# Optimization experiments

Measured on AMD Instinct MI355X. Metric: run time of the kernel, lower is better.

Reference implementation:

```python
import jax, jax.numpy as jnp
import numpy as np

B, S = 2, 1024
ENC_IN, MARK_IN = 21, 4
PRED_LEN, C_OUT = 96, 21
E = 512                 # embedding_dim
INNER = 2 * E           # proj_factor=2.0 (library default; Model does not pass it)
NH = 8                  # mLSTM heads
DH = INNER // NH        # 128
K = 4                   # causal conv1d kernel
BS = 4                  # qkv_proj_blocksize
NHP = INNER // BS       # 256 block-diagonal proj heads
NB = 4                  # num_blocks
EPS = 1e-5


def setup_inputs() -> dict:
    key = jax.random.key(0)
    ks = jax.random.split(key, 24)
    it = iter(range(24))
    def n(shape, s=0.02):
        return jax.random.normal(ks[next(it)], shape, jnp.float32) * s
    return {
        "x_enc": n((B, S, ENC_IN), 1.0),
        "x_mark_enc": n((B, S, MARK_IN), 1.0),
        "x_dec": n((B, PRED_LEN, ENC_IN), 1.0),
        "x_mark_dec": n((B, PRED_LEN, MARK_IN), 1.0),
        "emb_W": n((ENC_IN + MARK_IN, E), 0.05),
        "emb_b": jnp.zeros((E,), jnp.float32),
        "ln_w": jnp.ones((NB, E), jnp.float32),
        "up_W": n((NB, E, 2 * INNER)),
        "conv_W": n((NB, INNER, K), 0.1),
        "conv_b": jnp.zeros((NB, INNER), jnp.float32),
        "q_W": n((NB, NHP, BS, BS), 0.1),
        "k_W": n((NB, NHP, BS, BS), 0.1),
        "v_W": n((NB, NHP, BS, BS), 0.1),
        "ig_W": n((NB, 3 * INNER, NH)),
        "ig_b": jnp.zeros((NB, NH), jnp.float32),
        "fg_W": n((NB, 3 * INNER, NH)),
        "fg_b": jnp.tile(jnp.linspace(3.0, 6.0, NH, dtype=jnp.float32), (NB, 1)),
        "skip": jnp.ones((NB, INNER), jnp.float32),
        "onorm_w": jnp.ones((NB, INNER), jnp.float32),
        "down_W": n((NB, INNER, E)),
        "post_ln_w": jnp.ones((E,), jnp.float32),
        "head_W": n((E, C_OUT), 0.05),
        "head_b": jnp.zeros((C_OUT,), jnp.float32),
    }


def _ln(x, w):
    mu = jnp.mean(x, -1, keepdims=True)
    var = jnp.var(x, -1, keepdims=True)
    return (x - mu) * jax.lax.rsqrt(var + EPS) * w


def _headwise(x, w):
    # block-diagonal LinearHeadwiseExpand: (B,S,INNER) with (NHP,BS,BS) blocks
    xh = x.reshape(x.shape[0], x.shape[1], NHP, BS)
    return jnp.einsum('bshd,hod->bsho', xh, w).reshape(x.shape)


def _block(x, lw, uW, cW, cb, qW, kW, vW, igW, igb, fgW, fgb, sk, ow, dW):
    xn = _ln(x, lw)
    up = xn @ uW                                  # (B,S,2*INNER)
    xm, z = up[..., :INNER], up[..., INNER:]
    # causal depthwise conv1d + SiLU
    xc = jax.lax.conv_general_dilated(
        xm.transpose(0, 2, 1), cW[:, None, :], (1,), [(K - 1, 0)],
        feature_group_count=INNER,
        dimension_numbers=('NCH', 'OIH', 'NCH')).transpose(0, 2, 1) + cb
    xc = jax.nn.silu(xc)
    q = _headwise(xc, qW)
    k = _headwise(xc, kW)
    v = _headwise(xm, vW)
    qkv = jnp.concatenate([q, k, v], -1)          # (B,S,3*INNER)
    ig = (qkv @ igW + igb).transpose(0, 2, 1)     # (B,NH,S)
    fg = (qkv @ fgW + fgb).transpose(0, 2, 1)
    qh = q.reshape(B, S, NH, DH).transpose(0, 2, 1, 3)
    kh = k.reshape(B, S, NH, DH).transpose(0, 2, 1, 3)
    vh = v.reshape(B, S, NH, DH).transpose(0, 2, 1, 3)
    # parallel stabilized mLSTM (exp-gated linear attention)
    log_f = jax.nn.log_sigmoid(fg)
    cs = jnp.cumsum(log_f, -1)                    # (B,NH,S)
    Mmat = cs[..., :, None] - cs[..., None, :]    # (B,NH,S,S) cumulative decay
    tri = jnp.tril(jnp.ones((S, S), bool))
    logD = jnp.where(tri, Mmat + ig[..., None, :], -jnp.inf)
    m = jnp.max(logD, -1, keepdims=True)          # row-wise stabilizer
    D = jnp.exp(logD - m)
    qk = jnp.einsum('bnsd,bntd->bnst', qh, kh) / (DH ** 0.5)
    C = qk * D
    norm = jnp.maximum(jnp.abs(jnp.sum(C, -1, keepdims=True)), jnp.exp(-m))
    h = jnp.einsum('bnst,bntd->bnsd', C / (norm + 1e-6), vh)
    # multi-head layernorm (groupnorm over DH per head), weight, no bias
    hn = (h - jnp.mean(h, -1, keepdims=True)) * jax.lax.rsqrt(jnp.var(h, -1, keepdims=True) + EPS)
    hn = hn.transpose(0, 2, 1, 3).reshape(B, S, INNER) * ow
    hs = (hn + sk * xc) * jax.nn.silu(z)          # learnable skip + output gate
    return x + hs @ dW                            # residual


def reference(x_enc, x_mark_enc, x_dec, x_mark_dec, emb_W, emb_b, ln_w, up_W,
              conv_W, conv_b, q_W, k_W, v_W, ig_W, ig_b, fg_W, fg_b, skip,
              onorm_w, down_W, post_ln_w, head_W, head_b):
    x = jnp.concatenate([x_enc, x_mark_enc], -1) @ emb_W + emb_b
    for i in range(NB):
        x = _block(x, ln_w[i], up_W[i], conv_W[i], conv_b[i], q_W[i], k_W[i],
                   v_W[i], ig_W[i], ig_b[i], fg_W[i], fg_b[i], skip[i],
                   onorm_w[i], down_W[i])
    x = _ln(x, post_ln_w)
    return x[:, -PRED_LEN:, :] @ head_W + head_b
```

## Files before the change

kernel.cpp:

```cpp
#include <hip/hip_runtime.h>
#include <hip/hip_bf16.h>

#define S_LEN 1024
#define E_DIM 512
#define INNER_D 1024
#define NHEAD 8
#define DHEAD 128

typedef unsigned short u16;
typedef unsigned int u32;
typedef __attribute__((ext_vector_type(8))) short short8;
typedef __attribute__((ext_vector_type(4))) float f32x4;

union S8 { short8 v; u16 u[8]; uint4 q; };

__device__ __forceinline__ u16 f2bf(float f) {
  u32 u = __float_as_uint(f);
  u32 r = u + 0x7FFFu + ((u >> 16) & 1u);
  return (u16)(r >> 16);
}
__device__ __forceinline__ float bf2f(u16 u) { return __uint_as_float(((u32)u) << 16); }

__device__ __forceinline__ void gload16(const u16* g, u16* l) {
  __builtin_amdgcn_global_load_lds((const __attribute__((address_space(1))) void*)g,
                                   (__attribute__((address_space(3))) void*)l, 16, 0, 0);
}

__device__ __forceinline__ void prep_transpose(
    const float* __restrict__ in, u16* __restrict__ out, int K, int N,
    int k0, int n0, int t, u16 (*T)[72])
{
  int kr = t >> 2, nseg = (t & 3) * 16;
  const float* src = in + (size_t)(k0 + kr) * N + n0 + nseg;
#pragma unroll
  for (int j = 0; j < 16; j++) T[kr][nseg + j] = f2bf(src[j]);
  __syncthreads();
  int nr = t >> 2, kseg = (t & 3) * 16;
  u32 u[8];
#pragma unroll
  for (int rr = 0; rr < 8; rr++) {
    u32 lo = T[kseg + 2 * rr][nr];
    u32 hi = T[kseg + 2 * rr + 1][nr];
    u[rr] = lo | (hi << 16);
  }
  u16* dst = out + (size_t)(n0 + nr) * K + k0 + kseg;
  uint4 w0 = {u[0], u[1], u[2], u[3]};
  uint4 w1 = {u[4], u[5], u[6], u[7]};
  *(uint4*)dst = w0;
  *(uint4*)(dst + 8) = w1;
}

__global__ __launch_bounds__(256) void prep_kernel(
    const float* __restrict__ up_W, u16* __restrict__ upWt,
    const float* __restrict__ down_W, u16* __restrict__ dnWt,
    const float* __restrict__ igW, const float* __restrict__ fgW,
    u16* __restrict__ ghi, u16* __restrict__ glo,
    const float* __restrict__ xe, const float* __restrict__ xmk,
    const float* __restrict__ eW, const float* __restrict__ eb,
    float* __restrict__ x)
{
  __shared__ u16 T[64][72];
  __shared__ float in_s[25];
  int id = blockIdx.x;
  int t = threadIdx.x;
  if (id < 1024) {
    int bx = id & 7, rest = id >> 3;
    int by = rest & 31, L = rest >> 5;
    prep_transpose(up_W + (size_t)L * 512 * 2048, upWt + (size_t)L * 1048576,
                   512, 2048, bx * 64, by * 64, t, T);
  } else if (id < 1536) {
    int id2 = id - 1024;
    int bx = id2 & 15, rest = id2 >> 4;
    int by = rest & 7, L = rest >> 3;
    prep_transpose(down_W + (size_t)L * 1024 * 512, dnWt + (size_t)L * 524288,
                   1024, 512, bx * 64, by * 64, t, T);
  } else if (id < 2304) {
    int id3 = id - 1536;
    int bx = id3 % 12, rest = id3 / 12;
    int n = rest & 15, L = rest >> 4;
    int k = bx * 256 + t;
    const float* W = ((n < 8) ? igW : fgW) + (size_t)L * 24576;
    float v = W[(size_t)k * 8 + (n & 7)];
    u16 h = f2bf(v);
    u16 l = f2bf(v - bf2f(h));
    size_t o = ((size_t)L * 16 + n) * 3072 + k;
    ghi[o] = h;
    glo[o] = l;
  } else {
    int row = id - 2304;
    if (t < 21) in_s[t] = xe[row * 21 + t];
    else if (t < 25) in_s[t] = xmk[row * 4 + t - 21];
    __syncthreads();
#pragma unroll
    for (int rep = 0; rep < 2; rep++) {
      int e = t + rep * 256;
      float acc = eb[e];
#pragma unroll
      for (int i = 0; i < 25; i++) acc += in_s[i] * eW[i * E_DIM + e];
      x[(size_t)row * E_DIM + e] = acc;
    }
  }
}

__global__ __launch_bounds__(256) void ln_kernel(
    const float* __restrict__ x, const float* __restrict__ w, u16* __restrict__ out)
{
  int row = blockIdx.x, tid = threadIdx.x;
  const float* xr = x + (size_t)row * E_DIM;
  float2 v = *(const float2*)(xr + tid * 2);
  float s = v.x + v.y, q = v.x * v.x + v.y * v.y;
#pragma unroll
  for (int off = 32; off; off >>= 1) { s += __shfl_xor(s, off); q += __shfl_xor(q, off); }
  __shared__ float ssum[4], ssq[4];
  int wv = tid >> 6;
  if ((tid & 63) == 0) { ssum[wv] = s; ssq[wv] = q; }
  __syncthreads();
  s = ssum[0] + ssum[1] + ssum[2] + ssum[3];
  q = ssq[0] + ssq[1] + ssq[2] + ssq[3];
  float mu = s * (1.f / E_DIM);
  float var = q * (1.f / E_DIM) - mu * mu;
  float rs = rsqrtf(var + 1e-5f);
  int e = tid * 2;
  ushort2 o;
  o.x = f2bf((v.x - mu) * rs * w[e]);
  o.y = f2bf((v.y - mu) * rs * w[e + 1]);
  *(ushort2*)(out + (size_t)row * E_DIM + e) = o;
}

__global__ __launch_bounds__(256) void lnhead_kernel(
    const float* __restrict__ x, const float* __restrict__ w,
    const float* __restrict__ hW, const float* __restrict__ hb,
    float* __restrict__ out)
{
  int ridx = blockIdx.x;
  int b = ridx / 96, r = ridx % 96;
  int row = b * S_LEN + (S_LEN - 96) + r;
  int tid = threadIdx.x;
  const float* xr = x + (size_t)row * E_DIM;
  float2 v = *(const float2*)(xr + tid * 2);
  float s = v.x + v.y, q = v.x * v.x + v.y * v.y;
#pragma unroll
  for (int off = 32; off; off >>= 1) { s += __shfl_xor(s, off); q += __shfl_xor(q, off); }
  __shared__ float ssum[4], ssq[4];
  __shared__ float lnv[512];
  __shared__ float part[8][32];
  int wv = tid >> 6;
  if ((tid & 63) == 0) { ssum[wv] = s; ssq[wv] = q; }
  __syncthreads();
  s = ssum[0] + ssum[1] + ssum[2] + ssum[3];
  q = ssq[0] + ssq[1] + ssq[2] + ssq[3];
  float mu = s * (1.f / E_DIM);
  float var = q * (1.f / E_DIM) - mu * mu;
  float rs = rsqrtf(var + 1e-5f);
  int e = tid * 2;
  lnv[e]     = (v.x - mu) * rs * w[e];
  lnv[e + 1] = (v.y - mu) * rs * w[e + 1];
  __syncthreads();
  int n = tid & 31, sl = tid >> 5;
  float p = 0.f;
  if (n < 21) {
#pragma unroll 8
    for (int kk = 0; kk < 64; kk++)
      p += lnv[sl * 64 + kk] * hW[(sl * 64 + kk) * 21 + n];
  }
  part[sl][n] = p;
  __syncthreads();
  if (tid < 21) {
    float acc = hb[tid];
#pragma unroll
    for (int j = 0; j < 8; j++) acc += part[j][tid];
    out[ridx * 21 + tid] = acc;
  }
}

__global__ __launch_bounds__(256) void gemm_bf16_split64(
    const u16* __restrict__ A, const u16* __restrict__ Bt,
    float* __restrict__ C0, u16* __restrict__ C1,
    int M, int N, int K, int split_col, int ldc)
{
  __shared__ u16 As0[128 * 32], As1[128 * 32], As2[128 * 32];
  __shared__ u16 Bs0[128 * 32], Bs1[128 * 32], Bs2[128 * 32];
  const int tid = threadIdx.x;
  const int row0 = blockIdx.y * 128, col0 = blockIdx.x * 128;
  const int wave = tid >> 6, lane = tid & 63;
  const int wr = wave >> 1, wc = wave & 1;
  const int lm = lane & 15, lq = lane >> 4;
  const int lr4 = lane >> 2;
  const int cg4 = (lane & 3) ^ (lr4 & 3);
  f32x4 acc[4][4] = {};
  const u16* Abase = A + (size_t)(row0 + lr4) * K + cg4 * 8;
  const u16* Bbase = Bt + (size_t)(col0 + lr4) * K + cg4 * 8;
  const int key = lm & 3;

#define STG_UP(AS, BS, K0) do { \
  _Pragma("unroll") for (int i = 0; i < 2; i++) \
    gload16(Abase + (size_t)((wave * 2 + i) * 16) * K + (K0), &AS[(wave * 2 + i) * 512]); \
  _Pragma("unroll") for (int i = 0; i < 2; i++) \
    gload16(Bbase + (size_t)((wave * 2 + i) * 16) * K + (K0), &BS[(wave * 2 + i) * 512]); \
} while (0)

#define CMP_UP(AS, BS) do { \
  short8 af[4], bfv[4]; \
  _Pragma("unroll") for (int i = 0; i < 4; i++) \
    af[i] = *(const short8*)&AS[(wr * 64 + i * 16 + lm) * 32 + ((lq ^ key) * 8)]; \
  _Pragma("unroll") for (int j = 0; j < 4; j++) \
    bfv[j] = *(const short8*)&BS[(wc * 64 + j * 16 + lm) * 32 + ((lq ^ key) * 8)]; \
  _Pragma("unroll") for (int i = 0; i < 4; i++) \
    _Pragma("unroll") for (int j = 0; j < 4; j++) \
      acc[i][j] = __builtin_amdgcn_mfma_f32_16x16x32_bf16(af[i], bfv[j], acc[i][j], 0, 0, 0); \
} while (0)

  STG_UP(As0, Bs0, 0);
  asm volatile("" ::: "memory");
  STG_UP(As1, Bs1, 32);
  asm volatile("" ::: "memory");
  STG_UP(As2, Bs2, 64);
#pragma unroll
  for (int t = 0; t < 16; t++) {
    if (t <= 13)      asm volatile("s_waitcnt vmcnt(8)" ::: "memory");
    else if (t == 14) asm volatile("s_waitcnt vmcnt(4)" ::: "memory");
    else              asm volatile("s_waitcnt vmcnt(0)" ::: "memory");
    __builtin_amdgcn_sched_barrier(0);
    __builtin_amdgcn_s_barrier();
    if ((t % 3) == 0)      CMP_UP(As0, Bs0);
    else if ((t % 3) == 1) CMP_UP(As1, Bs1);
    else                   CMP_UP(As2, Bs2);
    __builtin_amdgcn_s_barrier();
    if (t + 3 < 16) {
      if ((t % 3) == 0)      STG_UP(As0, Bs0, (t + 3) * 32);
      else if ((t % 3) == 1) STG_UP(As1, Bs1, (t + 3) * 32);
      else                   STG_UP(As2, Bs2, (t + 3) * 32);
    }
  }
#undef STG_UP
#undef CMP_UP

  const bool toC1 = (col0 >= split_col);
#pragma unroll
  for (int i = 0; i < 4; i++) {
#pragma unroll
    for (int j = 0; j < 4; j++) {
      int col = col0 - (toC1 ? split_col : 0) + wc * 64 + j * 16 + lm;
#pragma unroll
      for (int r = 0; r < 4; r++) {
        int row = row0 + wr * 64 + i * 16 + lq * 4 + r;
        if (toC1) C1[(size_t)row * ldc + col] = f2bf(acc[i][j][r]);
        else C0[(size_t)row * ldc + col] = acc[i][j][r];
      }
    }
  }
}

__global__ __launch_bounds__(256) void gemm_bf16_32(
    const u16* __restrict__ A, const u16* __restrict__ Bt,
    float* __restrict__ C, int M, int N, int K, int ldc)
{
  __shared__ u16 As0[64 * 64], As1[64 * 64], As2[64 * 64];
  __shared__ u16 Bs0[64 * 64], Bs1[64 * 64], Bs2[64 * 64];
  const int tid = threadIdx.x;
  const int row0 = blockIdx.y * 64, col0 = blockIdx.x * 64;
  const int wave = tid >> 6, lane = tid & 63;
  const int wr = wave >> 1, wc = wave & 1;
  const int lm = lane & 15, lq = lane >> 4;
  const int lr = lane >> 3;
  const int cg = (lane & 7) ^ lr;
  f32x4 acc[2][2] = {};
  const u16* Abase = A + (size_t)(row0 + lr) * K + cg * 8;
  const u16* Bbase = Bt + (size_t)(col0 + lr) * K + cg * 8;
  const int key = lm & 7;

#define STAGE_DN(AS, BS, K0) do { \
  _Pragma("unroll") for (int i = 0; i < 2; i++) \
    gload16(Abase + (size_t)((wave * 2 + i) * 8) * K + (K0), &AS[(wave * 2 + i) * 512]); \
  _Pragma("unroll") for (int j = 0; j < 2; j++) \
    gload16(Bbase + (size_t)((wave * 2 + j) * 8) * K + (K0), &BS[(wave * 2 + j) * 512]); \
} while (0)

#define COMPUTE_DN(AS, BS) do { \
  short8 af[2][2], bfv[2][2]; \
  _Pragma("unroll") for (int kc = 0; kc < 2; kc++) { \
    _Pragma("unroll") for (int i = 0; i < 2; i++) \
      af[kc][i] = *(const short8*)&AS[(wr * 32 + i * 16 + lm) * 64 + (((kc * 4 + lq) ^ key) * 8)]; \
    _Pragma("unroll") for (int j = 0; j < 2; j++) \
      bfv[kc][j] = *(const short8*)&BS[(wc * 32 + j * 16 + lm) * 64 + (((kc * 4 + lq) ^ key) * 8)]; \
  } \
  _Pragma("unroll") for (int kc = 0; kc < 2; kc++) \
    _Pragma("unroll") for (int i = 0; i < 2; i++) \
      _Pragma("unroll") for (int j = 0; j < 2; j++) \
        acc[i][j] = __builtin_amdgcn_mfma_f32_16x16x32_bf16(af[kc][i], bfv[kc][j], acc[i][j], 0, 0, 0); \
} while (0)

  STAGE_DN(As0, Bs0, 0);
  asm volatile("" ::: "memory");
  STAGE_DN(As1, Bs1, 64);
  asm volatile("" ::: "memory");
  STAGE_DN(As2, Bs2, 128);
#pragma unroll
  for (int t = 0; t < 16; t++) {
    if (t <= 13)      asm volatile("s_waitcnt vmcnt(8)" ::: "memory");
    else if (t == 14) asm volatile("s_waitcnt vmcnt(4)" ::: "memory");
    else              asm volatile("s_waitcnt vmcnt(0)" ::: "memory");
    __builtin_amdgcn_sched_barrier(0);
    __builtin_amdgcn_s_barrier();
    if ((t % 3) == 0)      COMPUTE_DN(As0, Bs0);
    else if ((t % 3) == 1) COMPUTE_DN(As1, Bs1);
    else                   COMPUTE_DN(As2, Bs2);
    __builtin_amdgcn_s_barrier();
    if (t + 3 < 16) {
      if ((t % 3) == 0)      STAGE_DN(As0, Bs0, (t + 3) * 64);
      else if ((t % 3) == 1) STAGE_DN(As1, Bs1, (t + 3) * 64);
      else                   STAGE_DN(As2, Bs2, (t + 3) * 64);
    }
  }
#undef STAGE_DN
#undef COMPUTE_DN

#pragma unroll
  for (int i = 0; i < 2; i++) {
#pragma unroll
    for (int j = 0; j < 2; j++) {
      int col = col0 + wc * 32 + j * 16 + lm;
#pragma unroll
      for (int r = 0; r < 4; r++) {
        int row = row0 + wr * 32 + i * 16 + lq * 4 + r;
        C[(size_t)row * ldc + col] += acc[i][j][r];
      }
    }
  }
}

__global__ __launch_bounds__(256) void convqkv_kernel(
    const float* __restrict__ xm,
    const float* __restrict__ cw, const float* __restrict__ cb,
    const float* __restrict__ qw, const float* __restrict__ kw, const float* __restrict__ vw,
    float* __restrict__ xc, u16* __restrict__ q, u16* __restrict__ k, u16* __restrict__ v,
    u16* __restrict__ vt)
{
  int r0 = blockIdx.x * 8;
  int s0 = r0 & (S_LEN - 1);
  int g = threadIdx.x;
  int c0 = g * 4;
  const float* base = xm + (size_t)r0 * INNER_D + c0;

  float4 xv[11];
#pragma unroll
  for (int j = 0; j < 11; j++) {
    int ts = s0 - 3 + j;
    float4 t = {0.f, 0.f, 0.f, 0.f};
    if (ts >= 0) t = *(const float4*)(base + (ptrdiff_t)(j - 3) * INNER_D);
    xv[j] = t;
  }
  float cwv[4][4];
#pragma unroll
  for (int c = 0; c < 4; c++)
#pragma unroll
    for (int kk = 0; kk < 4; kk++) cwv[c][kk] = cw[(c0 + c) * 4 + kk];
  float cbv[4] = {cb[c0], cb[c0 + 1], cb[c0 + 2], cb[c0 + 3]};
  const float* qg = qw + g * 16;
  const float* kg = kw + g * 16;
  const float* vg = vw + g * 16;
  float qwv[16], kwv[16], vwv[16];
#pragma unroll
  for (int i = 0; i < 16; i++) { qwv[i] = qg[i]; kwv[i] = kg[i]; vwv[i] = vg[i]; }

  u32 vt_pack[4][4];

#pragma unroll
  for (int i = 0; i < 8; i++) {
    float a0 = cbv[0], a1 = cbv[1], a2 = cbv[2], a3 = cbv[3];
#pragma unroll
    for (int kk = 0; kk < 4; kk++) {
      float4 xvv = xv[i + kk];
      a0 += xvv.x * cwv[0][kk];
      a1 += xvv.y * cwv[1][kk];
      a2 += xvv.z * cwv[2][kk];
      a3 += xvv.w * cwv[3][kk];
    }
    a0 = a0 / (1.f + __expf(-a0));
    a1 = a1 / (1.f + __expf(-a1));
    a2 = a2 / (1.f + __expf(-a2));
    a3 = a3 / (1.f + __expf(-a3));
    float4 accv = {a0, a1, a2, a3};
    *(float4*)(xc + (size_t)(r0 + i) * INNER_D + c0) = accv;

    float xcv[4] = {a0, a1, a2, a3};
    float xmv[4] = {xv[i + 3].x, xv[i + 3].y, xv[i + 3].z, xv[i + 3].w};
    ushort4 qs, ks, vs;
    u16* qp = (u16*)&qs; u16* kp = (u16*)&ks; u16* vp = (u16*)&vs;
#pragma unroll
    for (int o = 0; o < 4; o++) {
      float aq = 0.f, ak = 0.f, av = 0.f;
#pragma unroll
      for (int d = 0; d < 4; d++) {
        aq += xcv[d] * qwv[o * 4 + d];
        ak += xcv[d] * kwv[o * 4 + d];
        av += xmv[d] * vwv[o * 4 + d];
      }
      qp[o] = f2bf(aq); kp[o] = f2bf(ak);
      u16 vv = f2bf(av);
      vp[o] = vv;
      if ((i & 1) == 0) vt_pack[o][i >> 1] = (u32)vv;
      else              vt_pack[o][i >> 1] |= ((u32)vv) << 16;
    }
    size_t off = (size_t)(r0 + i) * INNER_D + c0;
    *(ushort4*)(q + off) = qs;
    *(ushort4*)(k + off) = ks;
    *(ushort4*)(v + off) = vs;
  }
  u16* vtb = vt + ((size_t)((r0 >> 10) * INNER_D + c0)) * S_LEN + s0;
#pragma unroll
  for (int c = 0; c < 4; c++) {
    uint4 wv4 = {vt_pack[c][0], vt_pack[c][1], vt_pack[c][2], vt_pack[c][3]};
    *(uint4*)(vtb + (size_t)c * S_LEN) = wv4;
  }
}

__global__ __launch_bounds__(256) void gates_mfma_kernel(
    const u16* __restrict__ q, const u16* __restrict__ k, const u16* __restrict__ v,
    const u16* __restrict__ whi, const u16* __restrict__ wlo,
    const float* __restrict__ igb, const float* __restrict__ fgb,
    float* __restrict__ ig, float* __restrict__ fg)
{
  const int blk2 = blockIdx.x;
  const int blk = blk2 >> 1, half = blk2 & 1;
  const int tid = threadIdx.x;
  const int wave = tid >> 6, lane = tid & 63;
  const int lm = lane & 15, lq = lane >> 4;
  const int grow = blk * 16 + lm;
  const u16* parts[3] = {q, k, v};
  f32x4 acc = {};
#pragma unroll 4
  for (int kc = 0; kc < 12; kc++) {
    int k0 = half * 1536 + wave * 384 + kc * 32;
    int part = k0 >> 10;
    int idx = (k0 & 1023) + lq * 8;
    S8 a, bh_, bl_;
    a.q = *(const uint4*)(parts[part] + (size_t)grow * INNER_D + idx);
    bh_.q = *(const uint4*)(whi + (size_t)lm * 3072 + k0 + lq * 8);
    bl_.q = *(const uint4*)(wlo + (size_t)lm * 3072 + k0 + lq * 8);
    __builtin_amdgcn_s_setprio(1);
    acc = __builtin_amdgcn_mfma_f32_16x16x32_bf16(a.v, bh_.v, acc, 0, 0, 0);
    acc = __builtin_amdgcn_mfma_f32_16x16x32_bf16(a.v, bl_.v, acc, 0, 0, 0);
    __builtin_amdgcn_s_setprio(0);
  }
  __shared__ float red[4][16][17];
#pragma unroll
  for (int r = 0; r < 4; r++) red[wave][lq * 4 + r][lm] = acc[r];
  __syncthreads();
  if (wave == 0) {
#pragma unroll
    for (int r = 0; r < 4; r++) {
      int row = lq * 4 + r;
      float sum = red[0][row][lm] + red[1][row][lm] + red[2][row][lm] + red[3][row][lm];
      int growr = blk * 16 + row;
      int b = growr >> 10, s = growr & (S_LEN - 1);
      if (lm < 8) {
        float bias = (half == 0) ? igb[lm] : 0.f;
        ig[half * 16384 + ((size_t)(b * NHEAD + lm) << 10) + s] = sum + bias;
      } else {
        float bias = (half == 0) ? fgb[lm - 8] : 0.f;
        fg[half * 16384 + ((size_t)(b * NHEAD + (lm - 8)) << 10) + s] = sum + bias;
      }
    }
  }
}

__global__ __launch_bounds__(1024) void scan_kernel(
    const float* __restrict__ ig, const float* __restrict__ fg,
    float* __restrict__ a, float* __restrict__ rm, float* __restrict__ enm)
{
  int bh = blockIdx.x;
  int t = threadIdx.x;
  int lane = t & 63, wv = t >> 6;
  __shared__ float sw[16];
  size_t o = ((size_t)bh << 10) + t;
  float f = fg[o] + fg[16384 + o];
  float lf = (f >= 0.f) ? -log1pf(__expf(-f)) : f - log1pf(__expf(f));
  float v = lf;
#pragma unroll
  for (int off = 1; off < 64; off <<= 1) {
    float u = __shfl_up(v, off);
    if (lane >= off) v += u;
  }
  if (lane == 63) sw[wv] = v;
  __syncthreads();
  float pre = 0.f;
  for (int w = 0; w < wv; w++) pre += sw[w];
  float cs = v + pre;
  float av = (ig[o] + ig[16384 + o]) - cs;
  a[o] = __expf(av);
  float m = av;
#pragma unroll
  for (int off = 1; off < 64; off <<= 1) {
    float u = __shfl_up(m, off);
    if (lane >= off) m = fmaxf(m, u);
  }
  __syncthreads();
  if (lane == 63) sw[wv] = m;
  __syncthreads();
  float pm = -3.4e38f;
  for (int w = 0; w < wv; w++) pm = fmaxf(pm, sw[w]);
  float rmx = fmaxf(m, pm);
  rm[o] = rmx;
  enm[o] = __expf(-(cs + rmx));
}

__device__ __constant__ int c_qp[15] = {7, 7, 7, 6, 6, 6, 5, 5, 4, 4, 3, 3, 2, 1, 0};
__device__ __constant__ int c_k0[15] = {0, 6,11, 0, 5,10, 0, 6, 0, 5, 0, 4, 0, 0, 0};
__device__ __constant__ int c_k1[15] = {6,11,16, 5,10,14, 6,12, 5,10, 4, 8, 6, 4, 2};
__device__ __constant__ int c_md[15] = {1, 2, 3, 1, 2, 3, 1, 2, 1, 2, 1, 2, 0, 0, 0};

#define HP_SLOT 1310720
#define SC_SLOT 10240

__global__ __launch_bounds__(512) void attn_mfma_kernel(
    const u16* __restrict__ qhg, const u16* __restrict__ khg, const u16* __restrict__ vtg,
    const float* __restrict__ a_arr, const float* __restrict__ rm_arr, const float* __restrict__ enm_arr,
    const float* __restrict__ xc, const u16* __restrict__ zh,
    const float* __restrict__ skip, const float* __restrict__ onw,
    u16* __restrict__ hs, float* __restrict__ hpart, float* __restrict__ scpart)
{
  const int bh = blockIdx.x;
  const int job = blockIdx.y;
  const int qp = c_qp[job], k0t = c_k0[job], k1t = c_k1[job], mode = c_md[job];
  const int b = bh >> 3, h = bh & 7;
  const int s0 = qp * 128;
  const int tid = threadIdx.x;
  const int wave = tid >> 6, lane = tid & 63;
  const int lm = lane & 15, lq = lane >> 4;
  const size_t rowbase = (size_t)b * S_LEN;
  const int c0 = h * DHEAD;

  __shared__ u16 Ks0[64 * 128], Ks1[64 * 128];
  __shared__ u16 Vt0[128 * 64], Vt1[128 * 64];
  __shared__ u16 Ws[128 * 72];

  short8 aq[4];
  {
    const u16* qpp = qhg + (rowbase + s0 + wave * 16 + lm) * INNER_D + c0 + lq * 8;
#pragma unroll
    for (int kc = 0; kc < 4; kc++) {
      S8 tmp; tmp.q = *(const uint4*)(qpp + kc * 32);
      aq[kc] = tmp.v;
    }
  }
  const float scale = 0.08838834764831845f;
  float rmv[4], er[4];
#pragma unroll
  for (int r = 0; r < 4; r++) {
    rmv[r] = rm_arr[(size_t)bh * S_LEN + s0 + wave * 16 + lq * 4 + r];
    er[r] = scale * __expf(-rmv[r]);
  }

  f32x4 accH[8] = {};
  float sc_acc[4] = {0.f, 0.f, 0.f, 0.f};
  const int lr16 = lane >> 4;
  const int ls16 = lane & 15;
  const int lr8 = lane >> 3;
  const int cgv = (lane & 7) ^ lr8;
  const u16* vtbase = vtg + ((size_t)b * INNER_D + c0) * S_LEN;

  float ae0[4], ae1[4];

#define PREF(KS, VS, AE, T0) do { \
  _Pragma("unroll") for (int j = 0; j < 2; j++) { \
    int rK = (wave * 2 + j) * 4 + lr16; \
    int cgk = ls16 ^ (rK & 7); \
    gload16(khg + (rowbase + (T0) + rK) * INNER_D + c0 + cgk * 8, &KS[(wave * 2 + j) * 512]); \
  } \
  _Pragma("unroll") for (int j = 0; j < 2; j++) { \
    int rV = (wave * 2 + j) * 8 + lr8; \
    gload16(vtbase + (size_t)rV * S_LEN + (T0) + cgv * 8, &VS[(wave * 2 + j) * 512]); \
  } \
  _Pragma("unroll") for (int cb = 0; cb < 4; cb++) \
    AE[cb] = a_arr[(size_t)bh * S_LEN + (T0) + cb * 16 + lm]; \
} while (0)

#define QK_STEP(KS, PACC) do { \
  __builtin_amdgcn_s_setprio(1); \
  _Pragma("unroll") for (int kc = 0; kc < 4; kc++) \
    _Pragma("unroll") for (int cb = 0; cb < 4; cb++) { \
      short8 bk = *(const short8*)&KS[(cb * 16 + lm) * 128 + (((kc * 4 + lq) ^ (lm & 7)) * 8)]; \
      PACC[cb] = __builtin_amdgcn_mfma_f32_16x16x32_bf16(aq[kc], bk, PACC[cb], 0, 0, 0); \
    } \
  __builtin_amdgcn_s_setprio(0); \
} while (0)

#define W_PV(AE, VT, T0, PACC) do { \
  float wpart[4] = {0.f, 0.f, 0.f, 0.f}; \
  _Pragma("unroll") for (int cb = 0; cb < 4; cb++) { \
    int colg = (T0) + cb * 16 + lm; \
    float ec = AE[cb]; \
    _Pragma("unroll") for (int r = 0; r < 4; r++) { \
      int rowg = s0 + wave * 16 + lq * 4 + r; \
      float wv = PACC[cb][r] * ec * er[r]; \
      if (colg > rowg) wv = 0.f; \
      wpart[r] += wv; \
      Ws[(wave * 16 + lq * 4 + r) * 72 + cb * 16 + lm] = f2bf(wv); \
    } \
  } \
  _Pragma("unroll") for (int r = 0; r < 4; r++) { \
    float sr = wpart[r]; \
    sr += __shfl_xor(sr, 1); sr += __shfl_xor(sr, 2); \
    sr += __shfl_xor(sr, 4); sr += __shfl_xor(sr, 8); \
    sc_acc[r] += sr; \
  } \
  __builtin_amdgcn_s_setprio(1); \
  _Pragma("unroll") for (int kc = 0; kc < 2; kc++) { \
    short8 aw = *(const short8*)&Ws[(wave * 16 + lm) * 72 + kc * 32 + lq * 8]; \
    _Pragma("unroll") for (int nb = 0; nb < 8; nb++) { \
      short8 bv = *(const short8*)&VT[(nb * 16 + lm) * 64 + (((kc * 4 + lq) ^ (lm & 7)) * 8)]; \
      accH[nb] = __builtin_amdgcn_mfma_f32_16x16x32_bf16(aw, bv, accH[nb], 0, 0, 0); \
    } \
  } \
  __builtin_amdgcn_s_setprio(0); \
} while (0)

  int kt = k0t;
  PREF(Ks0, Vt0, ae0, kt * 64);
  asm volatile("" ::: "memory");
  if (kt + 1 < k1t) PREF(Ks1, Vt1, ae1, (kt + 1) * 64);

  while (true) {
    {
      if (kt + 1 < k1t) asm volatile("s_waitcnt vmcnt(8)" ::: "memory");
      else              asm volatile("s_waitcnt vmcnt(0)" ::: "memory");
      __builtin_amdgcn_sched_barrier(0);
      __builtin_amdgcn_s_barrier();
      f32x4 pacc[4] = {};
      QK_STEP(Ks0, pacc);
      W_PV(ae0, Vt0, kt * 64, pacc);
      __builtin_amdgcn_s_barrier();
      if (kt + 2 < k1t) PREF(Ks0, Vt0, ae0, (kt + 2) * 64);
      kt++;
      if (kt >= k1t) break;
    }
    {
      if (kt + 1 < k1t) asm volatile("s_waitcnt vmcnt(8)" ::: "memory");
      else              asm volatile("s_waitcnt vmcnt(0)" ::: "memory");
      __builtin_amdgcn_sched_barrier(0);
      __builtin_amdgcn_s_barrier();
      f32x4 pacc[4] = {};
      QK_STEP(Ks1, pacc);
      W_PV(ae1, Vt1, kt * 64, pacc);
      __builtin_amdgcn_s_barrier();
      if (kt + 2 < k1t) PREF(Ks1, Vt1, ae1, (kt + 2) * 64);
      kt++;
      if (kt >= k1t) break;
    }
  }
#undef PREF
#undef QK_STEP
#undef W_PV

  if (mode != 0) {
    int slot = mode - 1;
    int qr = qp - 3;
    float* Hp = hpart + (size_t)slot * HP_SLOT + ((size_t)(bh * 5 + qr)) * 16384;
    float* sp = scpart + slot * SC_SLOT + (bh * 5 + qr) * 128;
#pragma unroll
    for (int r = 0; r < 4; r++) {
      int row = wave * 16 + lq * 4 + r;
      if (lm == 0) sp[row] = sc_acc[r];
#pragma unroll
      for (int nb = 0; nb < 8; nb++)
        Hp[row * 128 + nb * 16 + lm] = accH[nb][r];
    }
    return;
  }

  float inv[4], muv[4], rsv[4];
#pragma unroll
  for (int r = 0; r < 4; r++) {
    int rowg = s0 + wave * 16 + lq * 4 + r;
    float nrm = fmaxf(fabsf(sc_acc[r]), enm_arr[(size_t)bh * S_LEN + rowg]);
    inv[r] = 1.f / (nrm + 1e-6f);
  }
#pragma unroll
  for (int r = 0; r < 4; r++) {
    float s = 0.f, qq = 0.f;
#pragma unroll
    for (int nb = 0; nb < 8; nb++) {
      float hv = accH[nb][r] * inv[r];
      accH[nb][r] = hv;
      s += hv; qq += hv * hv;
    }
    s += __shfl_xor(s, 1); s += __shfl_xor(s, 2); s += __shfl_xor(s, 4); s += __shfl_xor(s, 8);
    qq += __shfl_xor(qq, 1); qq += __shfl_xor(qq, 2); qq += __shfl_xor(qq, 4); qq += __shfl_xor(qq, 8);
    float mu = s * (1.f / DHEAD);
    float var = qq * (1.f / DHEAD) - mu * mu;
    muv[r] = mu;
    rsv[r] = rsqrtf(var + 1e-5f);
  }
  float ow[8], sk[8];
#pragma unroll
  for (int nb = 0; nb < 8; nb++) {
    ow[nb] = onw[c0 + nb * 16 + lm];
    sk[nb] = skip[c0 + nb * 16 + lm];
  }
#pragma unroll
  for (int r = 0; r < 4; r++) {
    int rowg = s0 + wave * 16 + lq * 4 + r;
    size_t base = (rowbase + rowg) * INNER_D + c0;
#pragma unroll
    for (int nb = 0; nb < 8; nb++) {
      int d = nb * 16 + lm;
      float xcv = xc[base + d];
      float zv = bf2f(zh[base + d]);
      float hn = (accH[nb][r] - muv[r]) * rsv[r] * ow[nb] + sk[nb] * xcv;
      float o = hn * (zv / (1.f + __expf(-zv)));
      hs[base + d] = f2bf(o);
    }
  }
}

__global__ __launch_bounds__(256) void attn_combine_kernel(
    const float* __restrict__ hpart, const float* __restrict__ scpart,
    const float* __restrict__ enm,
    const float* __restrict__ xc, const u16* __restrict__ zh,
    const float* __restrict__ skip, const float* __restrict__ onw,
    u16* __restrict__ hs)
{
  int wave = threadIdx.x >> 6, lane = threadIdx.x & 63;
  int gid = blockIdx.x * 4 + wave;
  int bh = gid / 640;
  int rr = gid % 640;
  int qr = rr >> 7, row = rr & 127;
  int b = bh >> 3, hh = bh & 7;
  int s = (qr + 3) * 128 + row;
  int nsl = (qr >= 3) ? 3 : 2;
  size_t off = (((size_t)(bh * 5 + qr)) * 128 + row) * 128 + lane * 2;
  int sidx = (bh * 5 + qr) * 128 + row;
  float hx = 0.f, hy = 0.f, sc = 0.f;
  for (int sl = 0; sl < nsl; sl++) {
    float2 hp = *(const float2*)(hpart + (size_t)sl * HP_SLOT + off);
    hx += hp.x; hy += hp.y;
    sc += scpart[sl * SC_SLOT + sidx];
  }
  float nrm = fmaxf(fabsf(sc), enm[(size_t)bh * S_LEN + s]);
  float inv = 1.f / (nrm + 1e-6f);
  hx *= inv; hy *= inv;
  float sm = hx + hy, sq = hx * hx + hy * hy;
#pragma unroll
  for (int off2 = 32; off2; off2 >>= 1) { sm += __shfl_xor(sm, off2); sq += __shfl_xor(sq, off2); }
  float mu = sm * (1.f / DHEAD);
  float var = sq * (1.f / DHEAD) - mu * mu;
  float rs = rsqrtf(var + 1e-5f);
  int c0 = hh * DHEAD + lane * 2;
  size_t base = ((size_t)(b * S_LEN + s)) * INNER_D + c0;
  float2 xc2 = *(const float2*)(xc + base);
  ushort2 z2u = *(const ushort2*)(zh + base);
  float z2x = bf2f(z2u.x), z2y = bf2f(z2u.y);
  float skx = skip[c0], sky = skip[c0 + 1];
  float owx = onw[c0],  owy = onw[c0 + 1];
  ushort2 o;
  o.x = f2bf(((hx - mu) * rs * owx + skx * xc2.x) * (z2x / (1.f + __expf(-z2x))));
  o.y = f2bf(((hy - mu) * rs * owy + sky * xc2.y) * (z2y / (1.f + __expf(-z2y))));
  *(ushort2*)(hs + base) = o;
}

extern "C" void kernel_launch(void* const* d_in, const int* in_sizes, int n_in,
                              void* d_out, int out_size, void* d_ws, size_t ws_size,
                              hipStream_t stream)
{
  const float* x_enc   = (const float*)d_in[0];
  const float* x_mark  = (const float*)d_in[1];
  const float* emb_W   = (const float*)d_in[4];
  const float* emb_b   = (const float*)d_in[5];
  const float* ln_w    = (const float*)d_in[6];
  const float* up_W    = (const float*)d_in[7];
  const float* conv_W  = (const float*)d_in[8];
  const float* conv_b  = (const float*)d_in[9];
  const float* q_W     = (const float*)d_in[10];
  const float* k_W     = (const float*)d_in[11];
  const float* v_W     = (const float*)d_in[12];
  const float* ig_W    = (const float*)d_in[13];
  const float* ig_b    = (const float*)d_in[14];
  const float* fg_W    = (const float*)d_in[15];
  const float* fg_b    = (const float*)d_in[16];
  const float* skip_w  = (const float*)d_in[17];
  const float* onorm_w = (const float*)d_in[18];
  const float* down_W  = (const float*)d_in[19];
  const float* post_ln = (const float*)d_in[20];
  const float* head_W  = (const float*)d_in[21];
  const float* head_b  = (const float*)d_in[22];

  float* p = (float*)d_ws;
  float* x    = p; p += 1048576;
  float* xm   = p; p += 2097152;
  float* xc   = p; p += 2097152;
  float* igb_ = p; p += 32768;
  float* fgb_ = p; p += 32768;
  float* ab   = p; p += 16384;
  float* rmb  = p; p += 16384;
  float* enmb = p; p += 16384;
  u16* qhb = (u16*)p; p += 1048576;
  u16* khb = (u16*)p; p += 1048576;
  u16* vhb = (u16*)p; p += 1048576;
  u16* zh  = (u16*)p; p += 1048576;
  u16* xnh = (u16*)p; p += 524288;
  u16* upWtA = (u16*)p; p += 2097152;
  u16* dnWtA = (u16*)p; p += 1048576;
  u16* gtwH = (u16*)p; p += 98304;
  u16* gtwL = (u16*)p; p += 98304;
  float* hpart = p; p += 3932160;
  float* scpart = p; p += 32768;
  u16* vtg = (u16*)p; p += 1048576;
  u16* hsbh = (u16*)xm;

  prep_kernel<<<4352, 256, 0, stream>>>(
      up_W, upWtA, down_W, dnWtA, ig_W, fg_W, gtwH, gtwL,
      x_enc, x_mark, emb_W, emb_b, x);

  for (int L = 0; L < 4; L++) {
    ln_kernel<<<2048, 256, 0, stream>>>(x, ln_w + L * 512, xnh);
    gemm_bf16_split64<<<dim3(16, 16), 256, 0, stream>>>(
        xnh, upWtA + (size_t)L * 1048576, xm, zh, 2048, 2048, 512, 1024, 1024);
    convqkv_kernel<<<256, 256, 0, stream>>>(
        xm, conv_W + L * 4096, conv_b + L * 1024,
        q_W + L * 4096, k_W + L * 4096, v_W + L * 4096,
        xc, qhb, khb, vhb, vtg);
    gates_mfma_kernel<<<256, 256, 0, stream>>>(
        qhb, khb, vhb, gtwH + (size_t)L * 49152, gtwL + (size_t)L * 49152,
        ig_b + L * 8, fg_b + L * 8, igb_, fgb_);
    scan_kernel<<<16, 1024, 0, stream>>>(igb_, fgb_, ab, rmb, enmb);
    attn_mfma_kernel<<<dim3(16, 15), 512, 0, stream>>>(
        qhb, khb, vtg, ab, rmb, enmb, xc, zh,
        skip_w + L * 1024, onorm_w + L * 1024, hsbh, hpart, scpart);
    attn_combine_kernel<<<2560, 256, 0, stream>>>(
        hpart, scpart, enmb, xc, zh, skip_w + L * 1024, onorm_w + L * 1024, hsbh);
    gemm_bf16_32<<<dim3(8, 32), 256, 0, stream>>>(
        hsbh, dnWtA + (size_t)L * 524288, x, 2048, 512, 1024, 512);
  }

  lnhead_kernel<<<192, 256, 0, stream>>>(x, post_ln, head_W, head_b, (float*)d_out);
}
```

Measured before the change: 428.8 us.

## Double GEMM K-tiles, compute mLSTM row sums via MFMA, skip mask on off-diagonal tiles

Both projection GEMMs now stage K-tiles twice as deep (64 and 128), with new XOR swizzles and half as many pipeline iterations and barriers. In the attention kernel, the per-row sum of the decay-weighted scores is computed with an extra MFMA against a ones vector, replacing the shuffle reductions. The causal mask is applied only on tiles that touch the diagonal. The row sum now uses bf16-rounded weights, which slightly changes the normaliser. The larger LDS footprint may reduce occupancy.

```diff
diff --git a/kernel.cpp b/kernel.cpp
--- a/kernel.cpp
+++ b/kernel.cpp
@@ -178,47 +178,49 @@
     float* __restrict__ C0, u16* __restrict__ C1,
     int M, int N, int K, int split_col, int ldc)
 {
-  __shared__ u16 As0[128 * 32], As1[128 * 32], As2[128 * 32];
-  __shared__ u16 Bs0[128 * 32], Bs1[128 * 32], Bs2[128 * 32];
+  __shared__ u16 As0[128 * 64], As1[128 * 64], As2[128 * 64];
+  __shared__ u16 Bs0[128 * 64], Bs1[128 * 64], Bs2[128 * 64];
   const int tid = threadIdx.x;
   const int row0 = blockIdx.y * 128, col0 = blockIdx.x * 128;
   const int wave = tid >> 6, lane = tid & 63;
   const int wr = wave >> 1, wc = wave & 1;
   const int lm = lane & 15, lq = lane >> 4;
-  const int lr4 = lane >> 2;
-  const int cg4 = (lane & 3) ^ (lr4 & 3);
+  const int lr8 = lane >> 3;
+  const int cg8 = (lane & 7) ^ lr8;
   f32x4 acc[4][4] = {};
-  const u16* Abase = A + (size_t)(row0 + lr4) * K + cg4 * 8;
-  const u16* Bbase = Bt + (size_t)(col0 + lr4) * K + cg4 * 8;
-  const int key = lm & 3;
+  const u16* Abase = A + (size_t)(row0 + lr8) * K + cg8 * 8;
+  const u16* Bbase = Bt + (size_t)(col0 + lr8) * K + cg8 * 8;
+  const int key = lm & 7;
 
 #define STG_UP(AS, BS, K0) do { \
-  _Pragma("unroll") for (int i = 0; i < 2; i++) \
-    gload16(Abase + (size_t)((wave * 2 + i) * 16) * K + (K0), &AS[(wave * 2 + i) * 512]); \
-  _Pragma("unroll") for (int i = 0; i < 2; i++) \
-    gload16(Bbase + (size_t)((wave * 2 + i) * 16) * K + (K0), &BS[(wave * 2 + i) * 512]); \
+  _Pragma("unroll") for (int i = 0; i < 4; i++) \
+    gload16(Abase + (size_t)((wave * 4 + i) * 8) * K + (K0), &AS[(wave * 4 + i) * 512]); \
+  _Pragma("unroll") for (int i = 0; i < 4; i++) \
+    gload16(Bbase + (size_t)((wave * 4 + i) * 8) * K + (K0), &BS[(wave * 4 + i) * 512]); \
 } while (0)
 
 #define CMP_UP(AS, BS) do { \
-  short8 af[4], bfv[4]; \
-  _Pragma("unroll") for (int i = 0; i < 4; i++) \
-    af[i] = *(const short8*)&AS[(wr * 64 + i * 16 + lm) * 32 + ((lq ^ key) * 8)]; \
-  _Pragma("unroll") for (int j = 0; j < 4; j++) \
-    bfv[j] = *(const short8*)&BS[(wc * 64 + j * 16 + lm) * 32 + ((lq ^ key) * 8)]; \
-  _Pragma("unroll") for (int i = 0; i < 4; i++) \
+  _Pragma("unroll") for (int kc = 0; kc < 2; kc++) { \
+    short8 af[4], bfv[4]; \
+    _Pragma("unroll") for (int i = 0; i < 4; i++) \
+      af[i] = *(const short8*)&AS[(wr * 64 + i * 16 + lm) * 64 + (((kc * 4 + lq) ^ key) * 8)]; \
     _Pragma("unroll") for (int j = 0; j < 4; j++) \
-      acc[i][j] = __builtin_amdgcn_mfma_f32_16x16x32_bf16(af[i], bfv[j], acc[i][j], 0, 0, 0); \
+      bfv[j] = *(const short8*)&BS[(wc * 64 + j * 16 + lm) * 64 + (((kc * 4 + lq) ^ key) * 8)]; \
+    _Pragma("unroll") for (int i = 0; i < 4; i++) \
+      _Pragma("unroll") for (int j = 0; j < 4; j++) \
+        acc[i][j] = __builtin_amdgcn_mfma_f32_16x16x32_bf16(af[i], bfv[j], acc[i][j], 0, 0, 0); \
+  } \
 } while (0)
 
   STG_UP(As0, Bs0, 0);
   asm volatile("" ::: "memory");
-  STG_UP(As1, Bs1, 32);
+  STG_UP(As1, Bs1, 64);
   asm volatile("" ::: "memory");
-  STG_UP(As2, Bs2, 64);
-#pragma unroll
-  for (int t = 0; t < 16; t++) {
-    if (t <= 13)      asm volatile("s_waitcnt vmcnt(8)" ::: "memory");
-    else if (t == 14) asm volatile("s_waitcnt vmcnt(4)" ::: "memory");
+  STG_UP(As2, Bs2, 128);
+#pragma unroll
+  for (int t = 0; t < 8; t++) {
+    if (t <= 5)       asm volatile("s_waitcnt vmcnt(16)" ::: "memory");
+    else if (t == 6)  asm volatile("s_waitcnt vmcnt(8)" ::: "memory");
     else              asm volatile("s_waitcnt vmcnt(0)" ::: "memory");
     __builtin_amdgcn_sched_barrier(0);
     __builtin_amdgcn_s_barrier();
@@ -226,10 +228,10 @@
     else if ((t % 3) == 1) CMP_UP(As1, Bs1);
     else                   CMP_UP(As2, Bs2);
     __builtin_amdgcn_s_barrier();
-    if (t + 3 < 16) {
-      if ((t % 3) == 0)      STG_UP(As0, Bs0, (t + 3) * 32);
-      else if ((t % 3) == 1) STG_UP(As1, Bs1, (t + 3) * 32);
-      else                   STG_UP(As2, Bs2, (t + 3) * 32);
+    if (t + 3 < 8) {
+      if ((t % 3) == 0)      STG_UP(As0, Bs0, (t + 3) * 64);
+      else if ((t % 3) == 1) STG_UP(As1, Bs1, (t + 3) * 64);
+      else                   STG_UP(As2, Bs2, (t + 3) * 64);
     }
   }
 #undef STG_UP
@@ -255,50 +257,52 @@
     const u16* __restrict__ A, const u16* __restrict__ Bt,
     float* __restrict__ C, int M, int N, int K, int ldc)
 {
-  __shared__ u16 As0[64 * 64], As1[64 * 64], As2[64 * 64];
-  __shared__ u16 Bs0[64 * 64], Bs1[64 * 64], Bs2[64 * 64];
+  __shared__ u16 As0[64 * 128], As1[64 * 128], As2[64 * 128];
+  __shared__ u16 Bs0[64 * 128], Bs1[64 * 128], Bs2[64 * 128];
   const int tid = threadIdx.x;
   const int row0 = blockIdx.y * 64, col0 = blockIdx.x * 64;
   const int wave = tid >> 6, lane = tid & 63;
   const int wr = wave >> 1, wc = wave & 1;
   const int lm = lane & 15, lq = lane >> 4;
-  const int lr = lane >> 3;
-  const int cg = (lane & 7) ^ lr;
+  const int lr16 = lane >> 4;
+  const int ls16 = lane & 15;
   f32x4 acc[2][2] = {};
-  const u16* Abase = A + (size_t)(row0 + lr) * K + cg * 8;
-  const u16* Bbase = Bt + (size_t)(col0 + lr) * K + cg * 8;
-  const int key = lm & 7;
 
 #define STAGE_DN(AS, BS, K0) do { \
-  _Pragma("unroll") for (int i = 0; i < 2; i++) \
-    gload16(Abase + (size_t)((wave * 2 + i) * 8) * K + (K0), &AS[(wave * 2 + i) * 512]); \
-  _Pragma("unroll") for (int j = 0; j < 2; j++) \
-    gload16(Bbase + (size_t)((wave * 2 + j) * 8) * K + (K0), &BS[(wave * 2 + j) * 512]); \
+  _Pragma("unroll") for (int i = 0; i < 4; i++) { \
+    int rA = (wave * 4 + i) * 4 + lr16; \
+    int cgk = ls16 ^ (rA & 15); \
+    gload16(A + (size_t)(row0 + rA) * K + (K0) + cgk * 8, &AS[(wave * 4 + i) * 512]); \
+  } \
+  _Pragma("unroll") for (int i = 0; i < 4; i++) { \
+    int rB = (wave * 4 + i) * 4 + lr16; \
+    int cgk = ls16 ^ (rB & 15); \
+    gload16(Bt + (size_t)(col0 + rB) * K + (K0) + cgk * 8, &BS[(wave * 4 + i) * 512]); \
+  } \
 } while (0)
 
 #define COMPUTE_DN(AS, BS) do { \
-  short8 af[2][2], bfv[2][2]; \
-  _Pragma("unroll") for (int kc = 0; kc < 2; kc++) { \
+  _Pragma("unroll") for (int kc = 0; kc < 4; kc++) { \
+    short8 af[2], bfv[2]; \
     _Pragma("unroll") for (int i = 0; i < 2; i++) \
-      af[kc][i] = *(const short8*)&AS[(wr * 32 + i * 16 + lm) * 64 + (((kc * 4 + lq) ^ key) * 8)]; \
+      af[i] = *(const short8*)&AS[(wr * 32 + i * 16 + lm) * 128 + (((kc * 4 + lq) ^ lm) * 8)]; \
     _Pragma("unroll") for (int j = 0; j < 2; j++) \
-      bfv[kc][j] = *(const short8*)&BS[(wc * 32 + j * 16 + lm) * 64 + (((kc * 4 + lq) ^ key) * 8)]; \
-  } \
-  _Pragma("unroll") for (int kc = 0; kc < 2; kc++) \
+      bfv[j] = *(const short8*)&BS[(wc * 32 + j * 16 + lm) * 128 + (((kc * 4 + lq) ^ lm) * 8)]; \
     _Pragma("unroll") for (int i = 0; i < 2; i++) \
       _Pragma("unroll") for (int j = 0; j < 2; j++) \
-        acc[i][j] = __builtin_amdgcn_mfma_f32_16x16x32_bf16(af[kc][i], bfv[kc][j], acc[i][j], 0, 0, 0); \
+        acc[i][j] = __builtin_amdgcn_mfma_f32_16x16x32_bf16(af[i], bfv[j], acc[i][j], 0, 0, 0); \
+  } \
 } while (0)
 
   STAGE_DN(As0, Bs0, 0);
   asm volatile("" ::: "memory");
-  STAGE_DN(As1, Bs1, 64);
+  STAGE_DN(As1, Bs1, 128);
   asm volatile("" ::: "memory");
-  STAGE_DN(As2, Bs2, 128);
-#pragma unroll
-  for (int t = 0; t < 16; t++) {
-    if (t <= 13)      asm volatile("s_waitcnt vmcnt(8)" ::: "memory");
-    else if (t == 14) asm volatile("s_waitcnt vmcnt(4)" ::: "memory");
+  STAGE_DN(As2, Bs2, 256);
+#pragma unroll
+  for (int t = 0; t < 8; t++) {
+    if (t <= 5)       asm volatile("s_waitcnt vmcnt(16)" ::: "memory");
+    else if (t == 6)  asm volatile("s_waitcnt vmcnt(8)" ::: "memory");
     else              asm volatile("s_waitcnt vmcnt(0)" ::: "memory");
     __builtin_amdgcn_sched_barrier(0);
     __builtin_amdgcn_s_barrier();
@@ -306,10 +310,10 @@
     else if ((t % 3) == 1) COMPUTE_DN(As1, Bs1);
     else                   COMPUTE_DN(As2, Bs2);
     __builtin_amdgcn_s_barrier();
-    if (t + 3 < 16) {
-      if ((t % 3) == 0)      STAGE_DN(As0, Bs0, (t + 3) * 64);
-      else if ((t % 3) == 1) STAGE_DN(As1, Bs1, (t + 3) * 64);
-      else                   STAGE_DN(As2, Bs2, (t + 3) * 64);
+    if (t + 3 < 8) {
+      if ((t % 3) == 0)      STAGE_DN(As0, Bs0, (t + 3) * 128);
+      else if ((t % 3) == 1) STAGE_DN(As1, Bs1, (t + 3) * 128);
+      else                   STAGE_DN(As2, Bs2, (t + 3) * 128);
     }
   }
 #undef STAGE_DN
@@ -552,8 +556,13 @@
     er[r] = scale * __expf(-rmv[r]);
   }
 
+  S8 onesu;
+#pragma unroll
+  for (int j = 0; j < 8; j++) onesu.u[j] = 0x3F80;
+  const short8 ones8 = onesu.v;
+
   f32x4 accH[8] = {};
-  float sc_acc[4] = {0.f, 0.f, 0.f, 0.f};
+  f32x4 accS = {};
   const int lr16 = lane >> 4;
   const int ls16 = lane & 15;
   const int lr8 = lane >> 3;
@@ -586,28 +595,23 @@
   __builtin_amdgcn_s_setprio(0); \
 } while (0)
 
-#define W_PV(AE, VT, T0, PACC) do { \
-  float wpart[4] = {0.f, 0.f, 0.f, 0.f}; \
+#define W_PV(AE, VT, T0, PACC, MSK) do { \
   _Pragma("unroll") for (int cb = 0; cb < 4; cb++) { \
-    int colg = (T0) + cb * 16 + lm; \
     float ec = AE[cb]; \
     _Pragma("unroll") for (int r = 0; r < 4; r++) { \
-      int rowg = s0 + wave * 16 + lq * 4 + r; \
       float wv = PACC[cb][r] * ec * er[r]; \
-      if (colg > rowg) wv = 0.f; \
-      wpart[r] += wv; \
+      if (MSK) { \
+        int colg = (T0) + cb * 16 + lm; \
+        int rowg = s0 + wave * 16 + lq * 4 + r; \
+        if (colg > rowg) wv = 0.f; \
+      } \
       Ws[(wave * 16 + lq * 4 + r) * 72 + cb * 16 + lm] = f2bf(wv); \
     } \
-  } \
-  _Pragma("unroll") for (int r = 0; r < 4; r++) { \
-    float sr = wpart[r]; \
-    sr += __shfl_xor(sr, 1); sr += __shfl_xor(sr, 2); \
-    sr += __shfl_xor(sr, 4); sr += __shfl_xor(sr, 8); \
-    sc_acc[r] += sr; \
   } \
   __builtin_amdgcn_s_setprio(1); \
   _Pragma("unroll") for (int kc = 0; kc < 2; kc++) { \
     short8 aw = *(const short8*)&Ws[(wave * 16 + lm) * 72 + kc * 32 + lq * 8]; \
+    accS = __builtin_amdgcn_mfma_f32_16x16x32_bf16(aw, ones8, accS, 0, 0, 0); \
     _Pragma("unroll") for (int nb = 0; nb < 8; nb++) { \
       short8 bv = *(const short8*)&VT[(nb * 16 + lm) * 64 + (((kc * 4 + lq) ^ (lm & 7)) * 8)]; \
       accH[nb] = __builtin_amdgcn_mfma_f32_16x16x32_bf16(aw, bv, accH[nb], 0, 0, 0); \
@@ -629,7 +633,8 @@
       __builtin_amdgcn_s_barrier();
       f32x4 pacc[4] = {};
       QK_STEP(Ks0, pacc);
-      W_PV(ae0, Vt0, kt * 64, pacc);
+      bool msk = (kt * 64 >= s0);
+      W_PV(ae0, Vt0, kt * 64, pacc, msk);
       __builtin_amdgcn_s_barrier();
       if (kt + 2 < k1t) PREF(Ks0, Vt0, ae0, (kt + 2) * 64);
       kt++;
@@ -642,7 +647,8 @@
       __builtin_amdgcn_s_barrier();
       f32x4 pacc[4] = {};
       QK_STEP(Ks1, pacc);
-      W_PV(ae1, Vt1, kt * 64, pacc);
+      bool msk = (kt * 64 >= s0);
+      W_PV(ae1, Vt1, kt * 64, pacc, msk);
       __builtin_amdgcn_s_barrier();
       if (kt + 2 < k1t) PREF(Ks1, Vt1, ae1, (kt + 2) * 64);
       kt++;
@@ -661,7 +667,7 @@
 #pragma unroll
     for (int r = 0; r < 4; r++) {
       int row = wave * 16 + lq * 4 + r;
-      if (lm == 0) sp[row] = sc_acc[r];
+      if (lm == 0) sp[row] = accS[r];
 #pragma unroll
       for (int nb = 0; nb < 8; nb++)
         Hp[row * 128 + nb * 16 + lm] = accH[nb][r];
@@ -673,7 +679,7 @@
 #pragma unroll
   for (int r = 0; r < 4; r++) {
     int rowg = s0 + wave * 16 + lq * 4 + r;
-    float nrm = fmaxf(fabsf(sc_acc[r]), enm_arr[(size_t)bh * S_LEN + rowg]);
+    float nrm = fmaxf(fabsf(accS[r]), enm_arr[(size_t)bh * S_LEN + rowg]);
     inv[r] = 1.f / (nrm + 1e-6f);
   }
 #pragma unroll
```

Result: faster. 415.5 us (-3.1%).
